# Kernel optimization log

Measured on AMD Instinct MI355X. Metric: run time of the kernel, lower is better.

## Reference

```python
import jax, jax.numpy as jnp
import numpy as np

N, E, DIMS, IN_C, OUT_C = 50000, 800000, 5, 32, 32
NEG_SLOPE = 0.2


def setup_inputs() -> dict:
    key = jax.random.key(0)
    k1, k2, k3, k4, k5 = jax.random.split(key, 5)
    x = jax.random.normal(k1, (N, IN_C * DIMS), dtype=jnp.float32)
    edge_index = jax.random.randint(k2, (2, E), 0, N, dtype=jnp.int64)
    edge_attr = jax.random.normal(k3, (E, DIMS), dtype=jnp.float32)
    # per-dim EGATConv parameters, stacked over dims (heads=1, concat=False)
    W = jax.random.normal(k4, (DIMS, IN_C, OUT_C), dtype=jnp.float32) / np.sqrt(IN_C).astype(np.float32)
    att = jax.random.normal(k5, (DIMS, 2 * OUT_C + 1), dtype=jnp.float32) / np.sqrt(2 * OUT_C + 1).astype(np.float32)
    return {"x": x, "edge_index": edge_index, "edge_attr": edge_attr, "W": W, "att": att}


def reference(x, edge_index, edge_attr, W, att):
    n = x.shape[0]
    dims, out_c = W.shape[0], W.shape[2]
    # x.reshape(N, -1, dims): per-dim feature slice, then per-dim linear projection
    xr = x.reshape(n, -1, dims)                      # [N, IN_C, dims]
    h = jnp.einsum('nid,dio->ndo', xr, W)            # [N, dims, OUT_C]
    row, col = edge_index[0], edge_index[1]
    h_i = h[row]                                     # [E, dims, OUT_C] target
    h_j = h[col]                                     # [E, dims, OUT_C] source
    att_i = att[:, :out_c]                           # [dims, OUT_C]
    att_j = att[:, out_c:2 * out_c]                  # [dims, OUT_C]
    att_e = att[:, -1]                               # [dims]
    # attention logits from cat([h_i, h_j, edge_attr]) . att, per edge, per dim
    score = (jnp.einsum('edo,do->ed', h_i, att_i)
             + jnp.einsum('edo,do->ed', h_j, att_j)
             + edge_attr * att_e)                    # [E, dims]
    score = jax.nn.leaky_relu(score, NEG_SLOPE)
    # scatter-softmax over incoming edges of each target node
    smax = jax.lax.stop_gradient(jax.ops.segment_max(score, row, num_segments=n))
    escore = jnp.exp(score - smax[row])
    ssum = jax.ops.segment_sum(escore, row, num_segments=n)
    alpha = escore / (ssum[row] + 1e-16)             # [E, dims]
    # scatter-add aggregation of alpha-weighted source features
    out = jax.ops.segment_sum(alpha[:, :, None] * h_j, row, num_segments=n)  # [N, dims, OUT_C]
    out = out.reshape(n, dims * out_c)               # torch.cat(out_l, dim=-1)
    return out, alpha, edge_index
```

## Files before the change

### kernel.cpp

```cpp
#include <hip/hip_runtime.h>
#include <hip/hip_bf16.h>
#include <math.h>

#define N_NODES 50000
#define N_EDGES 800000
#define DIMS 5
#define IN_C 32
#define OUT_C 32
#define FEAT 160
#define ATT_LD 65
#define NEG_SLOPE 0.2f
#define BSHIFT 7
#define BROWS 128
#define NBUCK ((N_NODES + BROWS - 1) / BROWS)
#define CAP 2560
#define K1_EPB 4096
#define K1_BLOCKS ((N_EDGES + K1_EPB - 1) / K1_EPB)

__global__ __launch_bounds__(1024) void hist_kernel(
        const int* __restrict__ ei, float* __restrict__ fedge,
        int* __restrict__ ghist, unsigned short* __restrict__ lofs) {
    __shared__ int hist[NBUCK];
    int blk = blockIdx.x, t = threadIdx.x;
    if (t < NBUCK) hist[t] = 0;
    __syncthreads();
#pragma unroll
    for (int u = 0; u < 4; ++u) {
        int e = blk * K1_EPB + u * 1024 + t;
        if (e < N_EDGES) {
            int r = ei[e];
            int c = ei[N_EDGES + e];
            __builtin_nontemporal_store((float)r, &fedge[e]);
            __builtin_nontemporal_store((float)c, &fedge[N_EDGES + e]);
            int b = r >> BSHIFT;
            int lo = atomicAdd(&hist[b], 1);
            lofs[e] = (unsigned short)lo;
        }
    }
    __syncthreads();
    if (t < NBUCK) ghist[blk * NBUCK + t] = hist[t];
}

__global__ void colsum_kernel(const int* __restrict__ ghist, int* __restrict__ btot) {
    __shared__ int red[256];
    int b = blockIdx.x, t = threadIdx.x;
    int s = 0;
    for (int blk = t; blk < K1_BLOCKS; blk += 256) s += ghist[blk * NBUCK + b];
    red[t] = s;
    __syncthreads();
    for (int off = 128; off > 0; off >>= 1) {
        if (t < off) red[t] += red[t + off];
        __syncthreads();
    }
    if (t == 0) btot[b] = red[0];
}

__global__ void bscan2_kernel(const int* __restrict__ btot, int* __restrict__ bbase) {
    __shared__ int buf[512];
    int t = threadIdx.x;
    int v = (t < NBUCK) ? btot[t] : 0;
    buf[t] = v;
    __syncthreads();
    for (int off = 1; off < 512; off <<= 1) {
        int add = (t >= off) ? buf[t - off] : 0;
        __syncthreads();
        buf[t] += add;
        __syncthreads();
    }
    if (t < NBUCK) bbase[t] = buf[t] - v;
}

__global__ void colscan_kernel(const int* __restrict__ ghist, const int* __restrict__ bbase,
                               int* __restrict__ base2) {
    __shared__ int buf[256];
    int b = blockIdx.x, t = threadIdx.x;
    int v = (t < K1_BLOCKS) ? ghist[t * NBUCK + b] : 0;
    buf[t] = v;
    __syncthreads();
    for (int off = 1; off < 256; off <<= 1) {
        int add = (t >= off) ? buf[t - off] : 0;
        __syncthreads();
        buf[t] += add;
        __syncthreads();
    }
    if (t < K1_BLOCKS) base2[t * NBUCK + b] = bbase[b] + buf[t] - v;
}

__global__ __launch_bounds__(1024) void place_kernel(
        const int* __restrict__ ei, const unsigned short* __restrict__ lofs,
        const int* __restrict__ base2, int2* __restrict__ staged) {
    __shared__ int lbase[NBUCK];
    int blk = blockIdx.x, t = threadIdx.x;
    if (t < NBUCK) lbase[t] = base2[blk * NBUCK + t];
    __syncthreads();
#pragma unroll
    for (int u = 0; u < 4; ++u) {
        int e = blk * K1_EPB + u * 1024 + t;
        if (e < N_EDGES) {
            int r = ei[e];
            int c = ei[N_EDGES + e];
            int b = r >> BSHIFT;
            int pos = lbase[b] + (int)lofs[e];
            staged[pos] = make_int2(c, (e << BSHIFT) | (r & (BROWS - 1)));
        }
    }
}

__global__ __launch_bounds__(256) void build_kernel(
        const int2* __restrict__ staged, const int* __restrict__ btot,
        const int* __restrict__ bbase,
        int2* __restrict__ csr, int* __restrict__ rowStart) {
    __shared__ int2 sst[CAP];
    __shared__ int rcount[BROWS];
    __shared__ int rexcl[BROWS];
    __shared__ int sbuf[BROWS];
    int b = blockIdx.x;
    int t = threadIdx.x;
    int cnt  = btot[b];
    int base = bbase[b];
    const int2* sg = staged + base;
    for (int i = t; i < cnt; i += 256) sst[i] = sg[i];
    if (t < BROWS) rcount[t] = 0;
    __syncthreads();
    for (int i = t; i < cnt; i += 256) atomicAdd(&rcount[sst[i].y & (BROWS - 1)], 1);
    __syncthreads();
    if (t < BROWS) sbuf[t] = rcount[t];
    __syncthreads();
    for (int off = 1; off < BROWS; off <<= 1) {
        int add = (t < BROWS && t >= off) ? sbuf[t - off] : 0;
        __syncthreads();
        if (t < BROWS) sbuf[t] += add;
        __syncthreads();
    }
    if (t < BROWS) {
        rexcl[t] = sbuf[t] - rcount[t];
        int idx = b * BROWS + t;
        if (idx <= N_NODES) rowStart[idx] = base + rexcl[t];
        rcount[t] = 0;
    }
    __syncthreads();
    for (int i = t; i < cnt; i += 256) {
        int2 p = sst[i];
        int rl = p.y & (BROWS - 1);
        int lp = atomicAdd(&rcount[rl], 1);
        csr[base + rexcl[rl] + lp] = make_int2(p.x, p.y >> BSHIFT);
    }
}

__global__ __launch_bounds__(256) void hfused_kernel(
        const float* __restrict__ x, const float* __restrict__ W,
        const float* __restrict__ att,
        __hip_bfloat16* __restrict__ h2,
        float* __restrict__ ai, float* __restrict__ aj) {
    int idx = blockIdx.x * 256 + threadIdx.x;
    if (idx >= N_NODES * 8) return;
    int n = idx >> 3;
    int og = idx & 7;
    const float4* xr4 = (const float4*)(x + (size_t)n * FEAT);

    float acc[DIMS][4];
#pragma unroll
    for (int d = 0; d < DIMS; ++d)
#pragma unroll
        for (int q = 0; q < 4; ++q) acc[d][q] = 0.f;

#pragma unroll
    for (int ib = 0; ib < 8; ++ib) {
        float xs[20];
#pragma unroll
        for (int q = 0; q < 5; ++q) {
            float4 v = xr4[ib * 5 + q];
            xs[q * 4 + 0] = v.x; xs[q * 4 + 1] = v.y;
            xs[q * 4 + 2] = v.z; xs[q * 4 + 3] = v.w;
        }
#pragma unroll
        for (int ii = 0; ii < 4; ++ii) {
            int i = ib * 4 + ii;
#pragma unroll
            for (int d = 0; d < DIMS; ++d) {
                float xv = xs[ii * 5 + d];
                float4 wv = *(const float4*)(W + ((d * IN_C + i) * OUT_C) + og * 4);
                acc[d][0] += xv * wv.x; acc[d][1] += xv * wv.y;
                acc[d][2] += xv * wv.z; acc[d][3] += xv * wv.w;
            }
        }
    }

    __hip_bfloat16* hp = h2 + (size_t)n * FEAT + og * 4;
#pragma unroll
    for (int d = 0; d < DIMS; ++d) {
        union { __hip_bfloat16 h[4]; uint2 u; } pk;
        pk.h[0] = __float2bfloat16(acc[d][0]);
        pk.h[1] = __float2bfloat16(acc[d][1]);
        pk.h[2] = __float2bfloat16(acc[d][2]);
        pk.h[3] = __float2bfloat16(acc[d][3]);
        *(uint2*)(hp + d * OUT_C) = pk.u;
    }

    float pa[DIMS], pb[DIMS];
#pragma unroll
    for (int d = 0; d < DIMS; ++d) {
        const float* at = att + d * ATT_LD + og * 4;
        const float* bt = at + OUT_C;
        pa[d] = acc[d][0] * at[0] + acc[d][1] * at[1] + acc[d][2] * at[2] + acc[d][3] * at[3];
        pb[d] = acc[d][0] * bt[0] + acc[d][1] * bt[1] + acc[d][2] * bt[2] + acc[d][3] * bt[3];
    }
#pragma unroll
    for (int m = 1; m < 8; m <<= 1) {
#pragma unroll
        for (int d = 0; d < DIMS; ++d) {
            pa[d] += __shfl_xor(pa[d], m, 8);
            pb[d] += __shfl_xor(pb[d], m, 8);
        }
    }
    if (og == 0) {
#pragma unroll
        for (int d = 0; d < DIMS; ++d) {
            ai[n * DIMS + d] = pa[d];
            aj[n * DIMS + d] = pb[d];
        }
    }
}

__global__ void es_kernel(const int* __restrict__ ei,
                          const float* __restrict__ edge_attr,
                          const float* __restrict__ ai, const float* __restrict__ aj,
                          const float* __restrict__ att,
                          unsigned short* __restrict__ es2) {
    int idx = blockIdx.x * blockDim.x + threadIdx.x;
    if (idx >= N_EDGES * DIMS) return;
    int e = idx / DIMS;
    int d = idx - e * DIMS;
    int r = ei[e];
    int c = ei[N_EDGES + e];
    float s = ai[r * DIMS + d] + aj[c * DIMS + d]
            + edge_attr[idx] * att[d * ATT_LD + 2 * OUT_C];
    s = (s > 0.f) ? s : NEG_SLOPE * s;
    __hip_bfloat16 h = __float2bfloat16(__expf(s));
    es2[idx] = *(unsigned short*)&h;
}

__device__ inline float bf2f(unsigned short u) {
    return __uint_as_float(((unsigned)u) << 16);
}

__global__ __launch_bounds__(320) void out_kernel(
        const __hip_bfloat16* __restrict__ h2,
        const unsigned short* __restrict__ es2,
        const int2* __restrict__ csr,
        const int* __restrict__ rowStart,
        float* __restrict__ out, float* __restrict__ ssum) {
    int g = threadIdx.x / 40;
    int l = threadIdx.x - g * 40;
    int node = blockIdx.x * 8 + g;
    int d = l >> 3;
    int start = rowStart[node];
    int end   = rowStart[node + 1];
    float a0 = 0.f, a1 = 0.f, a2 = 0.f, a3 = 0.f, ss = 0.f;
    int k = start;
    for (; k + 7 < end; k += 8) {
        int2 ce[8]; float av[8]; uint2 hv[8];
#pragma unroll
        for (int u = 0; u < 8; ++u) ce[u] = csr[k + u];
#pragma unroll
        for (int u = 0; u < 8; ++u) av[u] = bf2f(es2[(size_t)ce[u].y * DIMS + d]);
#pragma unroll
        for (int u = 0; u < 8; ++u)
            hv[u] = *(const uint2*)(h2 + (size_t)ce[u].x * FEAT + l * 4);
#pragma unroll
        for (int u = 0; u < 8; ++u) {
            float a = av[u];
            ss += a;
            a0 += a * __uint_as_float(hv[u].x << 16);
            a1 += a * __uint_as_float(hv[u].x & 0xffff0000u);
            a2 += a * __uint_as_float(hv[u].y << 16);
            a3 += a * __uint_as_float(hv[u].y & 0xffff0000u);
        }
    }
    for (; k < end; ++k) {
        int2 ce = csr[k];
        float a = bf2f(es2[(size_t)ce.y * DIMS + d]);
        uint2 hv = *(const uint2*)(h2 + (size_t)ce.x * FEAT + l * 4);
        ss += a;
        a0 += a * __uint_as_float(hv.x << 16);
        a1 += a * __uint_as_float(hv.x & 0xffff0000u);
        a2 += a * __uint_as_float(hv.y << 16);
        a3 += a * __uint_as_float(hv.y & 0xffff0000u);
    }
    float inv = 1.f / (ss + 1e-16f);
    union { float f[4]; unsigned long long u[2]; } o;
    o.f[0] = a0 * inv; o.f[1] = a1 * inv; o.f[2] = a2 * inv; o.f[3] = a3 * inv;
    unsigned long long* op = (unsigned long long*)(out + (size_t)node * FEAT + l * 4);
    __builtin_nontemporal_store(o.u[0], op);
    __builtin_nontemporal_store(o.u[1], op + 1);
    if ((l & 7) == 0) ssum[node * DIMS + d] = ss;
}

__global__ void alpha_kernel(const int* __restrict__ ei,
                             const unsigned short* __restrict__ es2,
                             const float* __restrict__ ssum,
                             float* __restrict__ alpha_buf) {
    int idx = blockIdx.x * blockDim.x + threadIdx.x;
    if (idx >= N_EDGES * DIMS) return;
    int e = idx / DIMS;
    int d = idx - e * DIMS;
    int r = ei[e];
    float a = bf2f(es2[idx]) / (ssum[r * DIMS + d] + 1e-16f);
    __builtin_nontemporal_store(a, &alpha_buf[idx]);
}

extern "C" void kernel_launch(void* const* d_in, const int* in_sizes, int n_in,
                              void* d_out, int out_size, void* d_ws, size_t ws_size,
                              hipStream_t stream) {
    const float* x         = (const float*)d_in[0];
    const int*   ei        = (const int*)d_in[1];
    const float* edge_attr = (const float*)d_in[2];
    const float* W         = (const float*)d_in[3];
    const float* att       = (const float*)d_in[4];

    float* out_buf   = (float*)d_out;
    float* alpha_buf = out_buf + (size_t)N_NODES * FEAT;
    float* fedge     = alpha_buf + (size_t)N_EDGES * DIMS;

    char* wsb = (char*)d_ws;
    __hip_bfloat16* h2 = (__hip_bfloat16*)wsb;
    float* ai     = (float*)(wsb + 16000000);
    float* aj     = (float*)(wsb + 17000000);
    float* ssum   = (float*)(wsb + 18000000);
    int2* csr     = (int2*)(wsb + 19000000);
    int* rowStart = (int*)(wsb + 25400000);
    int* ghist    = (int*)(wsb + 25600064);
    int* base2    = (int*)(wsb + 25906624);
    int* btot     = (int*)(wsb + 26213184);
    int* bbase    = (int*)(wsb + 26214784);
    int2* staged  = (int2*)(wsb + 26216384);
    unsigned short* lofs = (unsigned short*)(wsb + 32616384);
    unsigned short* es2  = (unsigned short*)(wsb + 26216384);

    const int B = 256;

    hist_kernel<<<K1_BLOCKS, 1024, 0, stream>>>(ei, fedge, ghist, lofs);
    colsum_kernel<<<NBUCK, 256, 0, stream>>>(ghist, btot);
    bscan2_kernel<<<1, 512, 0, stream>>>(btot, bbase);
    colscan_kernel<<<NBUCK, 256, 0, stream>>>(ghist, bbase, base2);
    place_kernel<<<K1_BLOCKS, 1024, 0, stream>>>(ei, lofs, base2, staged);
    build_kernel<<<NBUCK, 256, 0, stream>>>(staged, btot, bbase, csr, rowStart);
    hfused_kernel<<<(N_NODES * 8 + B - 1) / B, B, 0, stream>>>(x, W, att, h2, ai, aj);
    es_kernel<<<(N_EDGES * DIMS + B - 1) / B, B, 0, stream>>>(ei, edge_attr, ai, aj, att, es2);
    out_kernel<<<N_NODES / 8, 320, 0, stream>>>(h2, es2, csr, rowStart, out_buf, ssum);
    alpha_kernel<<<(N_EDGES * DIMS + B - 1) / B, B, 0, stream>>>(ei, es2, ssum, alpha_buf);
}
```

Measured before the change: 170.2 us.

## Fuse edge scoring into placement, degree-sort nodes per bucket, stage in output buffer

Merges the separate edge-score kernel into the CSR placement kernel, which already reads the edge indices, so ei is read one time fewer and one launch disappears. The build kernel now counting-sorts the rows of each bucket by degree and emits a node permutation plus (start, degree) pairs. The aggregation kernel walks nodes in that order so that groups in a block get similar work, and it reads the CSR with nontemporal loads. Staging buffers move into the not-yet-written alpha output region and the projection kernel is launched earlier, at the cost of an extra indirection and some extra shared-memory scans.

After: 189.3 us. 11.2% more time.

```diff
diff --git a/kernel.cpp b/kernel.cpp
--- a/kernel.cpp
+++ b/kernel.cpp
@@ -13,6 +13,7 @@
 #define BSHIFT 7
 #define BROWS 128
 #define NBUCK ((N_NODES + BROWS - 1) / BROWS)
+#define NSLOTS (NBUCK * BROWS)
 #define CAP 2560
 #define K1_EPB 4096
 #define K1_BLOCKS ((N_EDGES + K1_EPB - 1) / K1_EPB)
@@ -86,12 +87,18 @@
     if (t < K1_BLOCKS) base2[t * NBUCK + b] = bbase[b] + buf[t] - v;
 }
 
-__global__ __launch_bounds__(1024) void place_kernel(
+__global__ __launch_bounds__(1024) void place_es_kernel(
         const int* __restrict__ ei, const unsigned short* __restrict__ lofs,
-        const int* __restrict__ base2, int2* __restrict__ staged) {
+        const int* __restrict__ base2,
+        const float* __restrict__ edge_attr,
+        const float* __restrict__ ai, const float* __restrict__ aj,
+        const float* __restrict__ att,
+        int2* __restrict__ staged, unsigned short* __restrict__ es2) {
     __shared__ int lbase[NBUCK];
+    __shared__ float satte[DIMS];
     int blk = blockIdx.x, t = threadIdx.x;
     if (t < NBUCK) lbase[t] = base2[blk * NBUCK + t];
+    if (t < DIMS) satte[t] = att[t * ATT_LD + 2 * OUT_C];
     __syncthreads();
 #pragma unroll
     for (int u = 0; u < 4; ++u) {
@@ -100,8 +107,17 @@
             int r = ei[e];
             int c = ei[N_EDGES + e];
             int b = r >> BSHIFT;
-            int pos = lbase[b] + (int)lofs[e];
-            staged[pos] = make_int2(c, (e << BSHIFT) | (r & (BROWS - 1)));
+            staged[lbase[b] + (int)lofs[e]] = make_int2(c, (e << BSHIFT) | (r & (BROWS - 1)));
+            const float* air = ai + r * DIMS;
+            const float* ajr = aj + c * DIMS;
+            const float* ea  = edge_attr + (size_t)e * DIMS;
+#pragma unroll
+            for (int d = 0; d < DIMS; ++d) {
+                float s = air[d] + ajr[d] + ea[d] * satte[d];
+                s = (s > 0.f) ? s : NEG_SLOPE * s;
+                __hip_bfloat16 h = __float2bfloat16(__expf(s));
+                es2[(size_t)e * DIMS + d] = *(unsigned short*)&h;
+            }
         }
     }
 }
@@ -109,11 +125,12 @@
 __global__ __launch_bounds__(256) void build_kernel(
         const int2* __restrict__ staged, const int* __restrict__ btot,
         const int* __restrict__ bbase,
-        int2* __restrict__ csr, int* __restrict__ rowStart) {
+        int2* __restrict__ csr, int2* __restrict__ rs2, int* __restrict__ nodeperm) {
     __shared__ int2 sst[CAP];
     __shared__ int rcount[BROWS];
     __shared__ int rexcl[BROWS];
     __shared__ int sbuf[BROWS];
+    __shared__ int h64[64], b64[64], c64[64];
     int b = blockIdx.x;
     int t = threadIdx.x;
     int cnt  = btot[b];
@@ -121,10 +138,12 @@
     const int2* sg = staged + base;
     for (int i = t; i < cnt; i += 256) sst[i] = sg[i];
     if (t < BROWS) rcount[t] = 0;
+    if (t < 64) { h64[t] = 0; c64[t] = 0; }
     __syncthreads();
     for (int i = t; i < cnt; i += 256) atomicAdd(&rcount[sst[i].y & (BROWS - 1)], 1);
     __syncthreads();
-    if (t < BROWS) sbuf[t] = rcount[t];
+    int deg = (t < BROWS) ? rcount[t] : 0;
+    if (t < BROWS) sbuf[t] = deg;
     __syncthreads();
     for (int off = 1; off < BROWS; off <<= 1) {
         int add = (t < BROWS && t >= off) ? sbuf[t - off] : 0;
@@ -132,10 +151,25 @@
         if (t < BROWS) sbuf[t] += add;
         __syncthreads();
     }
+    int key = (deg > 63) ? 63 : deg;
     if (t < BROWS) {
-        rexcl[t] = sbuf[t] - rcount[t];
-        int idx = b * BROWS + t;
-        if (idx <= N_NODES) rowStart[idx] = base + rexcl[t];
+        rexcl[t] = sbuf[t] - deg;
+        atomicAdd(&h64[key], 1);
+    }
+    __syncthreads();
+    if (t < 64) b64[t] = h64[t];
+    __syncthreads();
+    for (int off = 1; off < 64; off <<= 1) {
+        int add = (t < 64 && t >= off) ? b64[t - off] : 0;
+        __syncthreads();
+        if (t < 64) b64[t] += add;
+        __syncthreads();
+    }
+    if (t < BROWS) {
+        int rk = atomicAdd(&c64[key], 1);
+        int slot = b * BROWS + (b64[key] - h64[key]) + rk;
+        nodeperm[slot] = b * BROWS + t;
+        rs2[slot] = make_int2(base + rexcl[t], deg);
         rcount[t] = 0;
     }
     __syncthreads();
@@ -222,24 +256,6 @@
     }
 }
 
-__global__ void es_kernel(const int* __restrict__ ei,
-                          const float* __restrict__ edge_attr,
-                          const float* __restrict__ ai, const float* __restrict__ aj,
-                          const float* __restrict__ att,
-                          unsigned short* __restrict__ es2) {
-    int idx = blockIdx.x * blockDim.x + threadIdx.x;
-    if (idx >= N_EDGES * DIMS) return;
-    int e = idx / DIMS;
-    int d = idx - e * DIMS;
-    int r = ei[e];
-    int c = ei[N_EDGES + e];
-    float s = ai[r * DIMS + d] + aj[c * DIMS + d]
-            + edge_attr[idx] * att[d * ATT_LD + 2 * OUT_C];
-    s = (s > 0.f) ? s : NEG_SLOPE * s;
-    __hip_bfloat16 h = __float2bfloat16(__expf(s));
-    es2[idx] = *(unsigned short*)&h;
-}
-
 __device__ inline float bf2f(unsigned short u) {
     return __uint_as_float(((unsigned)u) << 16);
 }
@@ -248,25 +264,34 @@
         const __hip_bfloat16* __restrict__ h2,
         const unsigned short* __restrict__ es2,
         const int2* __restrict__ csr,
-        const int* __restrict__ rowStart,
+        const int2* __restrict__ rs2,
+        const int* __restrict__ nodeperm,
         float* __restrict__ out, float* __restrict__ ssum) {
     int g = threadIdx.x / 40;
     int l = threadIdx.x - g * 40;
-    int node = blockIdx.x * 8 + g;
+    int slot = blockIdx.x * 8 + g;
+    int node = nodeperm[slot];
+    if (node >= N_NODES) return;
+    int2 se = rs2[slot];
+    int start = se.x;
+    int end   = se.x + se.y;
     int d = l >> 3;
-    int start = rowStart[node];
-    int end   = rowStart[node + 1];
     float a0 = 0.f, a1 = 0.f, a2 = 0.f, a3 = 0.f, ss = 0.f;
     int k = start;
     for (; k + 7 < end; k += 8) {
-        int2 ce[8]; float av[8]; uint2 hv[8];
-#pragma unroll
-        for (int u = 0; u < 8; ++u) ce[u] = csr[k + u];
-#pragma unroll
-        for (int u = 0; u < 8; ++u) av[u] = bf2f(es2[(size_t)ce[u].y * DIMS + d]);
+        int cc[8], ee[8]; float av[8]; uint2 hv[8];
+#pragma unroll
+        for (int u = 0; u < 8; ++u) {
+            unsigned long long rv =
+                __builtin_nontemporal_load((const unsigned long long*)(csr + k + u));
+            cc[u] = (int)(rv & 0xffffffffULL);
+            ee[u] = (int)(rv >> 32);
+        }
+#pragma unroll
+        for (int u = 0; u < 8; ++u) av[u] = bf2f(es2[(size_t)ee[u] * DIMS + d]);
 #pragma unroll
         for (int u = 0; u < 8; ++u)
-            hv[u] = *(const uint2*)(h2 + (size_t)ce[u].x * FEAT + l * 4);
+            hv[u] = *(const uint2*)(h2 + (size_t)cc[u] * FEAT + l * 4);
 #pragma unroll
         for (int u = 0; u < 8; ++u) {
             float a = av[u];
@@ -322,31 +347,33 @@
     float* alpha_buf = out_buf + (size_t)N_NODES * FEAT;
     float* fedge     = alpha_buf + (size_t)N_EDGES * DIMS;
 
+    int2* staged = (int2*)alpha_buf;
+    unsigned short* lofs = (unsigned short*)((char*)alpha_buf + 6400000);
+
     char* wsb = (char*)d_ws;
     __hip_bfloat16* h2 = (__hip_bfloat16*)wsb;
     float* ai     = (float*)(wsb + 16000000);
     float* aj     = (float*)(wsb + 17000000);
     float* ssum   = (float*)(wsb + 18000000);
     int2* csr     = (int2*)(wsb + 19000000);
-    int* rowStart = (int*)(wsb + 25400000);
-    int* ghist    = (int*)(wsb + 25600064);
-    int* base2    = (int*)(wsb + 25906624);
-    int* btot     = (int*)(wsb + 26213184);
-    int* bbase    = (int*)(wsb + 26214784);
-    int2* staged  = (int2*)(wsb + 26216384);
-    unsigned short* lofs = (unsigned short*)(wsb + 32616384);
-    unsigned short* es2  = (unsigned short*)(wsb + 26216384);
+    int* ghist    = (int*)(wsb + 25400000);
+    int* base2    = (int*)(wsb + 25710000);
+    int* btot     = (int*)(wsb + 26020000);
+    int* bbase    = (int*)(wsb + 26022000);
+    int2* rs2     = (int2*)(wsb + 26024000);
+    int* nodeperm = (int*)(wsb + 26425000);
+    unsigned short* es2 = (unsigned short*)(wsb + 26626000);
 
     const int B = 256;
 
     hist_kernel<<<K1_BLOCKS, 1024, 0, stream>>>(ei, fedge, ghist, lofs);
+    hfused_kernel<<<(N_NODES * 8 + B - 1) / B, B, 0, stream>>>(x, W, att, h2, ai, aj);
     colsum_kernel<<<NBUCK, 256, 0, stream>>>(ghist, btot);
     bscan2_kernel<<<1, 512, 0, stream>>>(btot, bbase);
     colscan_kernel<<<NBUCK, 256, 0, stream>>>(ghist, bbase, base2);
-    place_kernel<<<K1_BLOCKS, 1024, 0, stream>>>(ei, lofs, base2, staged);
-    build_kernel<<<NBUCK, 256, 0, stream>>>(staged, btot, bbase, csr, rowStart);
-    hfused_kernel<<<(N_NODES * 8 + B - 1) / B, B, 0, stream>>>(x, W, att, h2, ai, aj);
-    es_kernel<<<(N_EDGES * DIMS + B - 1) / B, B, 0, stream>>>(ei, edge_attr, ai, aj, att, es2);
-    out_kernel<<<N_NODES / 8, 320, 0, stream>>>(h2, es2, csr, rowStart, out_buf, ssum);
+    place_es_kernel<<<K1_BLOCKS, 1024, 0, stream>>>(ei, lofs, base2, edge_attr,
+                                                    ai, aj, att, staged, es2);
+    build_kernel<<<NBUCK, 256, 0, stream>>>(staged, btot, bbase, csr, rs2, nodeperm);
+    out_kernel<<<NSLOTS / 8, 320, 0, stream>>>(h2, es2, csr, rs2, nodeperm, out_buf, ssum);
     alpha_kernel<<<(N_EDGES * DIMS + B - 1) / B, B, 0, stream>>>(ei, es2, ssum, alpha_buf);
 }
```

## Fuse edge-score computation into CSR placement and pack scores into CSR entries

Applied to the files above, without the earlier changes.

Removes the separate es_kernel. The projection kernel now runs before placement, so place_kernel can compute the five exp'd leaky-relu edge scores as bf16 and pack them, together with the source index and local row, into a 16-byte staged record. build_kernel carries these records into the CSR. out_kernel then reads the scores directly from its CSR entry instead of doing a scattered gather from es2. alpha_kernel recomputes the scores in fp32 instead of reading the bf16 buffer. The price is a CSR twice as large, 64 KB of LDS per build block, staging scratch placed in the alpha output region, and duplicated exp work in alpha_kernel.

Measured after the change: 185.9 us. +9.3%, slower.

```diff
diff --git a/kernel.cpp b/kernel.cpp
--- a/kernel.cpp
+++ b/kernel.cpp
@@ -88,10 +88,16 @@
 
 __global__ __launch_bounds__(1024) void place_kernel(
         const int* __restrict__ ei, const unsigned short* __restrict__ lofs,
-        const int* __restrict__ base2, int2* __restrict__ staged) {
+        const int* __restrict__ base2,
+        const float* __restrict__ edge_attr,
+        const float* __restrict__ ai, const float* __restrict__ aj,
+        const float* __restrict__ att,
+        int4* __restrict__ staged) {
     __shared__ int lbase[NBUCK];
+    __shared__ float satte[DIMS];
     int blk = blockIdx.x, t = threadIdx.x;
     if (t < NBUCK) lbase[t] = base2[blk * NBUCK + t];
+    if (t < DIMS) satte[t] = att[t * ATT_LD + 2 * OUT_C];
     __syncthreads();
 #pragma unroll
     for (int u = 0; u < 4; ++u) {
@@ -99,18 +105,32 @@
         if (e < N_EDGES) {
             int r = ei[e];
             int c = ei[N_EDGES + e];
-            int b = r >> BSHIFT;
-            int pos = lbase[b] + (int)lofs[e];
-            staged[pos] = make_int2(c, (e << BSHIFT) | (r & (BROWS - 1)));
+            const float* air = ai + r * DIMS;
+            const float* ajr = aj + c * DIMS;
+            const float* ea  = edge_attr + (size_t)e * DIMS;
+            unsigned es[DIMS];
+#pragma unroll
+            for (int d = 0; d < DIMS; ++d) {
+                float s = air[d] + ajr[d] + ea[d] * satte[d];
+                s = (s > 0.f) ? s : NEG_SLOPE * s;
+                __hip_bfloat16 h = __float2bfloat16(__expf(s));
+                es[d] = (unsigned)*(unsigned short*)&h;
+            }
+            int4 st;
+            st.x = c;
+            st.y = (int)(es[0] | (es[1] << 16));
+            st.z = (int)(es[2] | (es[3] << 16));
+            st.w = (int)(es[4] | ((unsigned)(r & (BROWS - 1)) << 16));
+            staged[lbase[r >> BSHIFT] + (int)lofs[e]] = st;
         }
     }
 }
 
 __global__ __launch_bounds__(256) void build_kernel(
-        const int2* __restrict__ staged, const int* __restrict__ btot,
+        const int4* __restrict__ staged, const int* __restrict__ btot,
         const int* __restrict__ bbase,
-        int2* __restrict__ csr, int* __restrict__ rowStart) {
-    __shared__ int2 sst[CAP];
+        int4* __restrict__ csr, int* __restrict__ rowStart) {
+    __shared__ int4 sst[CAP];
     __shared__ int rcount[BROWS];
     __shared__ int rexcl[BROWS];
     __shared__ int sbuf[BROWS];
@@ -118,11 +138,12 @@
     int t = threadIdx.x;
     int cnt  = btot[b];
     int base = bbase[b];
-    const int2* sg = staged + base;
+    const int4* sg = staged + base;
     for (int i = t; i < cnt; i += 256) sst[i] = sg[i];
     if (t < BROWS) rcount[t] = 0;
     __syncthreads();
-    for (int i = t; i < cnt; i += 256) atomicAdd(&rcount[sst[i].y & (BROWS - 1)], 1);
+    for (int i = t; i < cnt; i += 256)
+        atomicAdd(&rcount[((unsigned)sst[i].w >> 16) & (BROWS - 1)], 1);
     __syncthreads();
     if (t < BROWS) sbuf[t] = rcount[t];
     __syncthreads();
@@ -140,10 +161,10 @@
     }
     __syncthreads();
     for (int i = t; i < cnt; i += 256) {
-        int2 p = sst[i];
-        int rl = p.y & (BROWS - 1);
+        int4 p = sst[i];
+        int rl = ((unsigned)p.w >> 16) & (BROWS - 1);
         int lp = atomicAdd(&rcount[rl], 1);
-        csr[base + rexcl[rl] + lp] = make_int2(p.x, p.y >> BSHIFT);
+        csr[base + rexcl[rl] + lp] = p;
     }
 }
 
@@ -222,11 +243,74 @@
     }
 }
 
-__global__ void es_kernel(const int* __restrict__ ei,
-                          const float* __restrict__ edge_attr,
-                          const float* __restrict__ ai, const float* __restrict__ aj,
-                          const float* __restrict__ att,
-                          unsigned short* __restrict__ es2) {
+__device__ inline float bf2f(unsigned short u) {
+    return __uint_as_float(((unsigned)u) << 16);
+}
+
+__global__ __launch_bounds__(320) void out_kernel(
+        const __hip_bfloat16* __restrict__ h2,
+        const int4* __restrict__ csr,
+        const int* __restrict__ rowStart,
+        float* __restrict__ out, float* __restrict__ ssum) {
+    int g = threadIdx.x / 40;
+    int l = threadIdx.x - g * 40;
+    int node = blockIdx.x * 8 + g;
+    int d = l >> 3;
+    int sh = (d & 1) << 4;
+    int start = rowStart[node];
+    int end   = rowStart[node + 1];
+    float a0 = 0.f, a1 = 0.f, a2 = 0.f, a3 = 0.f, ss = 0.f;
+    int k = start;
+    for (; k + 7 < end; k += 8) {
+        int4 ce[8]; float av[8]; uint2 hv[8];
+#pragma unroll
+        for (int u = 0; u < 8; ++u) ce[u] = csr[k + u];
+#pragma unroll
+        for (int u = 0; u < 8; ++u) {
+            unsigned wsel = (d < 2) ? (unsigned)ce[u].y
+                          : (d < 4) ? (unsigned)ce[u].z : (unsigned)ce[u].w;
+            av[u] = bf2f((unsigned short)((wsel >> sh) & 0xffffu));
+        }
+#pragma unroll
+        for (int u = 0; u < 8; ++u)
+            hv[u] = *(const uint2*)(h2 + (size_t)ce[u].x * FEAT + l * 4);
+#pragma unroll
+        for (int u = 0; u < 8; ++u) {
+            float a = av[u];
+            ss += a;
+            a0 += a * __uint_as_float(hv[u].x << 16);
+            a1 += a * __uint_as_float(hv[u].x & 0xffff0000u);
+            a2 += a * __uint_as_float(hv[u].y << 16);
+            a3 += a * __uint_as_float(hv[u].y & 0xffff0000u);
+        }
+    }
+    for (; k < end; ++k) {
+        int4 ce = csr[k];
+        unsigned wsel = (d < 2) ? (unsigned)ce.y
+                      : (d < 4) ? (unsigned)ce.z : (unsigned)ce.w;
+        float a = bf2f((unsigned short)((wsel >> sh) & 0xffffu));
+        uint2 hv = *(const uint2*)(h2 + (size_t)ce.x * FEAT + l * 4);
+        ss += a;
+        a0 += a * __uint_as_float(hv.x << 16);
+        a1 += a * __uint_as_float(hv.x & 0xffff0000u);
+        a2 += a * __uint_as_float(hv.y << 16);
+        a3 += a * __uint_as_float(hv.y & 0xffff0000u);
+    }
+    float inv = 1.f / (ss + 1e-16f);
+    union { float f[4]; unsigned long long u[2]; } o;
+    o.f[0] = a0 * inv; o.f[1] = a1 * inv; o.f[2] = a2 * inv; o.f[3] = a3 * inv;
+    unsigned long long* op = (unsigned long long*)(out + (size_t)node * FEAT + l * 4);
+    __builtin_nontemporal_store(o.u[0], op);
+    __builtin_nontemporal_store(o.u[1], op + 1);
+    if ((l & 7) == 0) ssum[node * DIMS + d] = ss;
+}
+
+__global__ void alpha_kernel(const int* __restrict__ ei,
+                             const float* __restrict__ edge_attr,
+                             const float* __restrict__ ai, const float* __restrict__ aj,
+                             const float* __restrict__ att,
+                             const float* __restrict__ ssum,
+                             float* __restrict__ alpha_buf) {
     int idx = blockIdx.x * blockDim.x + threadIdx.x;
     if (idx >= N_EDGES * DIMS) return;
     int e = idx / DIMS;
@@ -236,76 +320,7 @@
     float s = ai[r * DIMS + d] + aj[c * DIMS + d]
             + edge_attr[idx] * att[d * ATT_LD + 2 * OUT_C];
     s = (s > 0.f) ? s : NEG_SLOPE * s;
-    __hip_bfloat16 h = __float2bfloat16(__expf(s));
-    es2[idx] = *(unsigned short*)&h;
-}
-
-__device__ inline float bf2f(unsigned short u) {
-    return __uint_as_float(((unsigned)u) << 16);
-}
-
-__global__ __launch_bounds__(320) void out_kernel(
-        const __hip_bfloat16* __restrict__ h2,
-        const unsigned short* __restrict__ es2,
-        const int2* __restrict__ csr,
-        const int* __restrict__ rowStart,
-        float* __restrict__ out, float* __restrict__ ssum) {
-    int g = threadIdx.x / 40;
-    int l = threadIdx.x - g * 40;
-    int node = blockIdx.x * 8 + g;
-    int d = l >> 3;
-    int start = rowStart[node];
-    int end   = rowStart[node + 1];
-    float a0 = 0.f, a1 = 0.f, a2 = 0.f, a3 = 0.f, ss = 0.f;
-    int k = start;
-    for (; k + 7 < end; k += 8) {
-        int2 ce[8]; float av[8]; uint2 hv[8];
-#pragma unroll
-        for (int u = 0; u < 8; ++u) ce[u] = csr[k + u];
-#pragma unroll
-        for (int u = 0; u < 8; ++u) av[u] = bf2f(es2[(size_t)ce[u].y * DIMS + d]);
-#pragma unroll
-        for (int u = 0; u < 8; ++u)
-            hv[u] = *(const uint2*)(h2 + (size_t)ce[u].x * FEAT + l * 4);
-#pragma unroll
-        for (int u = 0; u < 8; ++u) {
-            float a = av[u];
-            ss += a;
-            a0 += a * __uint_as_float(hv[u].x << 16);
-            a1 += a * __uint_as_float(hv[u].x & 0xffff0000u);
-            a2 += a * __uint_as_float(hv[u].y << 16);
-            a3 += a * __uint_as_float(hv[u].y & 0xffff0000u);
-        }
-    }
-    for (; k < end; ++k) {
-        int2 ce = csr[k];
-        float a = bf2f(es2[(size_t)ce.y * DIMS + d]);
-        uint2 hv = *(const uint2*)(h2 + (size_t)ce.x * FEAT + l * 4);
-        ss += a;
-        a0 += a * __uint_as_float(hv.x << 16);
-        a1 += a * __uint_as_float(hv.x & 0xffff0000u);
-        a2 += a * __uint_as_float(hv.y << 16);
-        a3 += a * __uint_as_float(hv.y & 0xffff0000u);
-    }
-    float inv = 1.f / (ss + 1e-16f);
-    union { float f[4]; unsigned long long u[2]; } o;
-    o.f[0] = a0 * inv; o.f[1] = a1 * inv; o.f[2] = a2 * inv; o.f[3] = a3 * inv;
-    unsigned long long* op = (unsigned long long*)(out + (size_t)node * FEAT + l * 4);
-    __builtin_nontemporal_store(o.u[0], op);
-    __builtin_nontemporal_store(o.u[1], op + 1);
-    if ((l & 7) == 0) ssum[node * DIMS + d] = ss;
-}
-
-__global__ void alpha_kernel(const int* __restrict__ ei,
-                             const unsigned short* __restrict__ es2,
-                             const float* __restrict__ ssum,
-                             float* __restrict__ alpha_buf) {
-    int idx = blockIdx.x * blockDim.x + threadIdx.x;
-    if (idx >= N_EDGES * DIMS) return;
-    int e = idx / DIMS;
-    int d = idx - e * DIMS;
-    int r = ei[e];
-    float a = bf2f(es2[idx]) / (ssum[r * DIMS + d] + 1e-16f);
+    float a = __expf(s) / (ssum[r * DIMS + d] + 1e-16f);
     __builtin_nontemporal_store(a, &alpha_buf[idx]);
 }
 
@@ -322,31 +337,32 @@
     float* alpha_buf = out_buf + (size_t)N_NODES * FEAT;
     float* fedge     = alpha_buf + (size_t)N_EDGES * DIMS;
 
+    int4* staged = (int4*)alpha_buf;
+    unsigned short* lofs = (unsigned short*)((char*)alpha_buf + 12800000);
+
     char* wsb = (char*)d_ws;
     __hip_bfloat16* h2 = (__hip_bfloat16*)wsb;
     float* ai     = (float*)(wsb + 16000000);
     float* aj     = (float*)(wsb + 17000000);
     float* ssum   = (float*)(wsb + 18000000);
-    int2* csr     = (int2*)(wsb + 19000000);
-    int* rowStart = (int*)(wsb + 25400000);
-    int* ghist    = (int*)(wsb + 25600064);
-    int* base2    = (int*)(wsb + 25906624);
-    int* btot     = (int*)(wsb + 26213184);
-    int* bbase    = (int*)(wsb + 26214784);
-    int2* staged  = (int2*)(wsb + 26216384);
-    unsigned short* lofs = (unsigned short*)(wsb + 32616384);
-    unsigned short* es2  = (unsigned short*)(wsb + 26216384);
+    int4* csr     = (int4*)(wsb + 19000000);
+    int* ghist    = (int*)(wsb + 31800000);
+    int* base2    = (int*)(wsb + 32106560);
+    int* btot     = (int*)(wsb + 32413120);
+    int* bbase    = (int*)(wsb + 32414688);
+    int* rowStart = (int*)(wsb + 32416256);
 
     const int B = 256;
 
     hist_kernel<<<K1_BLOCKS, 1024, 0, stream>>>(ei, fedge, ghist, lofs);
+    hfused_kernel<<<(N_NODES * 8 + B - 1) / B, B, 0, stream>>>(x, W, att, h2, ai, aj);
     colsum_kernel<<<NBUCK, 256, 0, stream>>>(ghist, btot);
     bscan2_kernel<<<1, 512, 0, stream>>>(btot, bbase);
     colscan_kernel<<<NBUCK, 256, 0, stream>>>(ghist, bbase, base2);
-    place_kernel<<<K1_BLOCKS, 1024, 0, stream>>>(ei, lofs, base2, staged);
+    place_kernel<<<K1_BLOCKS, 1024, 0, stream>>>(ei, lofs, base2, edge_attr,
+                                                 ai, aj, att, staged);
     build_kernel<<<NBUCK, 256, 0, stream>>>(staged, btot, bbase, csr, rowStart);
-    hfused_kernel<<<(N_NODES * 8 + B - 1) / B, B, 0, stream>>>(x, W, att, h2, ai, aj);
-    es_kernel<<<(N_EDGES * DIMS + B - 1) / B, B, 0, stream>>>(ei, edge_attr, ai, aj, att, es2);
-    out_kernel<<<N_NODES / 8, 320, 0, stream>>>(h2, es2, csr, rowStart, out_buf, ssum);
-    alpha_kernel<<<(N_EDGES * DIMS + B - 1) / B, B, 0, stream>>>(ei, es2, ssum, alpha_buf);
-}
+    out_kernel<<<N_NODES / 8, 320, 0, stream>>>(h2, csr, rowStart, out_buf, ssum);
+    alpha_kernel<<<(N_EDGES * DIMS + B - 1) / B, B, 0, stream>>>(ei, edge_attr, ai, aj, att,
+                                                                 ssum, alpha_buf);
+}
```
